# Optimization experiments

Hardware: AMD Instinct MI355X
Metric: run time of the kernel (lower is better)

## Reference

```python
import jax, jax.numpy as jnp
import numpy as np
from jax import lax

# ---- module constants (mirror CorrelatedSphericalField.__init__) ----
NLAT = 361
NLON = 2 * NLAT
LMAX = NLAT            # number of degrees l
MMAX = NLAT + 1        # number of orders m = nlon//2 + 1
N_LATENT = 16
T_STEPS = 8
LENGTH_SCALE = 500_000.0
TIME_SCALE = 48.0
SIGMA = 0.3
DT = 6.0
R_EARTH = 6_371_000.0
PHI = float(np.exp(-DT / TIME_SCALE))
KT = (LENGTH_SCALE / R_EARTH) ** 2 / 2.0
FOUR_PI = float(4.0 * np.pi)


def _precompute_pct():
    """Associated Legendre tensor pct[m, l, k] for InverseRealSHT,
    equiangular grid, norm='backward' (orthonormal P / sqrt(4pi)), with
    Condon-Shortley phase -- matches torch_harmonics _precompute_legpoly(inverse=True)."""
    theta = np.linspace(0.0, np.pi, NLAT)      # equiangular incl. poles
    x = np.cos(theta)
    s = np.sin(theta)
    nmax = max(MMAX, LMAX)
    vdm = np.zeros((nmax, nmax, NLAT), dtype=np.float64)  # [m, l, lat]
    vdm[0, 0] = 1.0 / np.sqrt(4.0 * np.pi)
    for m in range(1, nmax):                    # diagonal P_m^m
        vdm[m, m] = np.sqrt((2.0 * m + 1.0) / (2.0 * m)) * s * vdm[m - 1, m - 1]
    for m in range(nmax - 1):                   # P_{m+1}^m
        vdm[m, m + 1] = np.sqrt(2.0 * m + 3.0) * x * vdm[m, m]
    for l in range(2, nmax):                    # three-term recurrence, vectorized over m
        ms = np.arange(l - 1)
        a = np.sqrt((4.0 * l * l - 1.0) / (l * l - ms * ms))[:, None]
        b = np.sqrt(((l - 1.0) ** 2 - ms * ms) / (4.0 * (l - 1.0) ** 2 - 1.0))[:, None]
        vdm[ms, l] = a * (x[None, :] * vdm[ms, l - 1] - b * vdm[ms, l - 2])
    vdm[1::2] *= -1.0                           # Condon-Shortley phase
    pct = vdm[:MMAX, :LMAX] / np.sqrt(4.0 * np.pi)  # norm='backward', inverse=True
    return jnp.asarray(pct, dtype=jnp.float32)


def _make_sigma_n():
    j = np.arange(1, NLAT, dtype=np.float64)
    denom = 2.0 * np.sum((2.0 * j + 1.0) * np.exp(-KT * j * (j + 1.0)))
    F0 = np.sqrt(SIGMA ** 2 * (1.0 - PHI ** 2) / denom)
    l = np.arange(NLAT, dtype=np.float64)
    prods = np.repeat((l * (l + 1.0))[:, None], MMAX, axis=1)   # (nlat, nlat+1)
    sn = np.tril(np.exp(-KT * prods / 2.0) * F0)                # keep m <= l
    return jnp.asarray(sn, dtype=jnp.float32)


def setup_inputs() -> dict:
    key = jax.random.key(0)
    k0, k1 = jax.random.split(key)
    sigma_n = _make_sigma_n()
    # initial stationary AR(1) coefficients: (1-phi^2)^{-1/2} * sigma_n * xi0
    xi0 = jax.random.normal(k0, (N_LATENT, LMAX, MMAX, 2), dtype=jnp.float32)
    coeff0 = (1.0 - PHI ** 2) ** (-0.5) * sigma_n[None, :, :, None] * xi0
    # pre-drawn innovations for the T AR(1) updates (real/imag stacked)
    xi = jax.random.normal(k1, (T_STEPS, N_LATENT, LMAX, MMAX, 2), dtype=jnp.float32)
    pct = _precompute_pct()
    x = jnp.zeros((T_STEPS,), dtype=jnp.int32)   # only x.shape[0] is used
    return {"x": x, "sigma_n": sigma_n, "coeff0": coeff0, "xi": xi, "pct": pct}


def reference(x, sigma_n, coeff0, xi, pct):
    T = x.shape[0]
    c0 = coeff0[..., 0] + 1j * coeff0[..., 1]    # (N, L, M) complex64
    xic = xi[..., 0] + 1j * xi[..., 1]           # (T, N, L, M) complex64

    # AR(1): emit coeff BEFORE update (matches the torch loop ordering)
    def step(c, xk):
        return PHI * c + sigma_n * xk, c

    _, coeffs = lax.scan(step, c0, xic[:T])      # (T, N, L, M)

    # inverse real SHT, batched over all T steps at once:
    # xs[..., k, m] = sum_l coeff[..., l, m] * pct[m, l, k]
    re = jnp.einsum('tnlm,mlk->tnkm', coeffs.real, pct)
    im = jnp.einsum('tnlm,mlk->tnkm', coeffs.imag, pct)
    xs = re + 1j * im                            # (T, N, nlat, mmax)
    out = jnp.fft.irfft(xs, n=NLON, axis=-1, norm='forward') * FOUR_PI
    return out.reshape(T, 1, 1, N_LATENT, NLAT, NLON)
```

## Files before the change

### kernel.cpp

```cpp
#include <hip/hip_runtime.h>
#include <math.h>

#define NLATC   361
#define NLONC   722
#define MMAXC   362
#define LMAXC   361
#define NLK     16
#define TSTEPS  8
#define LCUT    128
#define MCUT    128
#define MCK     256
#define TNK     46208
#define NPAD    768
#define KPAD    384
#define PHI_F   0.8824969025845955f
#define FOURPI  12.566370614359172f
#define ASCALE  1024.0f
#define OSCALE  0.0009765625f

typedef _Float16 half8 __attribute__((ext_vector_type(8)));
typedef float floatx4 __attribute__((ext_vector_type(4)));

__global__ __launch_bounds__(256) void k_basis2(_Float16* __restrict__ Bf) {
    int idx = blockIdx.x * 256 + threadIdx.x;
    int j = idx >> 8, mc = idx & 255;
    int m = mc >> 1, c = mc & 1;
    float v = 0.0f;
    if (j < NLONC) {
        int r = (m * j) % NLONC;
        float th = (float)r * (6.283185307179586f / 722.0f);
        float s, co;
        sincosf(th, &s, &co);
        float wq = (m == 0 ? 1.0f : 2.0f) * FOURPI;
        v = c ? (-wq * s) : (wq * co);
    }
    Bf[idx] = (_Float16)v;
}

__global__ __launch_bounds__(256) void k_scan(const float* __restrict__ coeff0,
                                              const float* __restrict__ sigma_n,
                                              const float* __restrict__ xi,
                                              float* __restrict__ cA) {
    int tid = blockIdx.x * 256 + threadIdx.x;
    int m = tid & 127;
    int l = (tid >> 7) & 127;
    int n = tid >> 14;
    float sg = sigma_n[(size_t)l * MMAXC + m];
    const float* c0p = coeff0 + (((size_t)n * LMAXC + l) * MMAXC + m) * 2;
    float cr = c0p[0], ci = c0p[1];
#pragma unroll
    for (int t = 0; t < TSTEPS; ++t) {
        size_t o = ((((size_t)t * NLK + n) * LCUT + l) * MCUT + m) * 2;
        cA[o] = cr; cA[o + 1] = ci;
        if (t < TSTEPS - 1) {
            const float* xp = xi + ((((size_t)t * NLK + n) * LMAXC + l) * MMAXC + m) * 2;
            cr = PHI_F * cr + sg * xp[0];
            ci = PHI_F * ci + sg * xp[1];
        }
    }
}

__global__ __launch_bounds__(256) void k_castA(const float* __restrict__ cA,
                                               _Float16* __restrict__ cB) {
    __shared__ _Float16 sm[64][66];
    int tx = threadIdx.x & 63, ty = threadIdx.x >> 6;
    int tnl0 = blockIdx.x * 64;
    int mc0  = blockIdx.y * 64;
    int tn = tnl0 >> 7, l0 = tnl0 & 127;
#pragma unroll
    for (int i = 0; i < 16; ++i) {
        int row = ty * 16 + i;
        sm[row][tx] = (_Float16)(cA[(size_t)(tnl0 + row) * MCK + mc0 + tx] * ASCALE);
    }
    __syncthreads();
#pragma unroll
    for (int i = 0; i < 16; ++i) {
        int rm = ty * 16 + i;
        int mc = mc0 + rm, m = mc >> 1, c = mc & 1;
        cB[((size_t)m * 256 + c * 128 + tn) * 128 + l0 + tx] = sm[tx][rm];
    }
}

__global__ __launch_bounds__(256) void k_transP(const float* __restrict__ pct,
                                                _Float16* __restrict__ pTf) {
    __shared__ _Float16 sm[64][66];
    int tx = threadIdx.x & 63, ty = threadIdx.x >> 6;
    int k0 = blockIdx.x * 64;
    int l0 = blockIdx.y * 64;
    int m  = blockIdx.z;
#pragma unroll
    for (int i = 0; i < 16; ++i) {
        int row = ty * 16 + i;
        int k = k0 + tx;
        sm[row][tx] = (k < NLATC)
            ? (_Float16)pct[((size_t)m * LMAXC + l0 + row) * NLATC + k] : (_Float16)0.0f;
    }
    __syncthreads();
#pragma unroll
    for (int i = 0; i < 16; ++i) {
        int kr = ty * 16 + i;
        pTf[((size_t)m * KPAD + k0 + kr) * 128 + l0 + tx] = sm[tx][kr];
    }
}

__global__ __launch_bounds__(256) void k_leg(const _Float16* __restrict__ cB,
                                             const _Float16* __restrict__ pTf,
                                             _Float16* __restrict__ xsTh) {
    __shared__ _Float16 As[256][40];
    __shared__ _Float16 Bs[64][40];
    int tid = threadIdx.x;
    int k0c = blockIdx.x * 64;
    int m   = blockIdx.y;
    int w = tid >> 6, lane = tid & 63, m16 = lane & 15, quad = lane >> 4;
    floatx4 acc[4][4];
#pragma unroll
    for (int i = 0; i < 4; ++i)
#pragma unroll
        for (int j = 0; j < 4; ++j) acc[i][j] = (floatx4)(0.0f);

    int lt0 = m & ~31;
    for (int lt = lt0; lt < 128; lt += 32) {
#pragma unroll
        for (int it = 0; it < 4; ++it) {
            int r = (tid >> 2) + 64 * it, lc = (tid & 3) * 8;
            *(half8*)&As[r][lc] = *(const half8*)&cB[((size_t)m * 256 + r) * 128 + lt + lc];
        }
        {
            int k = tid >> 2, lc = (tid & 3) * 8;
            *(half8*)&Bs[k][lc] = *(const half8*)&pTf[((size_t)m * KPAD + k0c + k) * 128 + lt + lc];
        }
        __syncthreads();
        half8 a[4], b[4];
#pragma unroll
        for (int i = 0; i < 4; ++i) a[i] = *(const half8*)&As[w * 64 + i * 16 + m16][quad * 8];
#pragma unroll
        for (int j = 0; j < 4; ++j) b[j] = *(const half8*)&Bs[j * 16 + m16][quad * 8];
#pragma unroll
        for (int i = 0; i < 4; ++i)
#pragma unroll
            for (int j = 0; j < 4; ++j)
                acc[i][j] = __builtin_amdgcn_mfma_f32_16x16x32_f16(a[i], b[j], acc[i][j], 0, 0, 0);
        __syncthreads();
    }
#pragma unroll
    for (int i = 0; i < 4; ++i)
#pragma unroll
        for (int j = 0; j < 4; ++j)
#pragma unroll
            for (int reg = 0; reg < 4; ++reg) {
                int r = w * 64 + i * 16 + quad * 4 + reg;
                int c = r >> 7, tn = r & 127;
                int k = k0c + j * 16 + m16;
                if (k < NLATC)
                    xsTh[(size_t)(2 * m + c) * TNK + tn * NLATC + k] = (_Float16)acc[i][j][reg];
            }
}

__global__ __launch_bounds__(256) void k_castXs(const _Float16* __restrict__ xsTh,
                                                _Float16* __restrict__ xsA) {
    __shared__ _Float16 sm[64][66];
    int tx = threadIdx.x & 63, ty = threadIdx.x >> 6;
    int t0  = blockIdx.x * 64;
    int mc0 = blockIdx.y * 64;
#pragma unroll
    for (int i = 0; i < 16; ++i) {
        int row = ty * 16 + i;
        sm[row][tx] = xsTh[(size_t)(mc0 + row) * TNK + t0 + tx];
    }
    __syncthreads();
#pragma unroll
    for (int i = 0; i < 16; ++i) {
        int row = ty * 16 + i;
        xsA[(size_t)(t0 + row) * MCK + mc0 + tx] = sm[tx][row];
    }
}

__global__ __launch_bounds__(256) void k_gemm2(const _Float16* __restrict__ A,
                                               const _Float16* __restrict__ Bf,
                                               float* __restrict__ C) {
    __shared__ _Float16 As[128][40];
    __shared__ _Float16 Bs[128][40];
    int tid = threadIdx.x;
    int row0 = blockIdx.x * 128;
    int j0   = blockIdx.y * 128;
    int w = tid >> 6, lane = tid & 63, m16 = lane & 15, quad = lane >> 4;
    int wr = (w & 1) * 64, wc = (w >> 1) * 64;
    floatx4 acc[4][4];
#pragma unroll
    for (int i = 0; i < 4; ++i)
#pragma unroll
        for (int j = 0; j < 4; ++j) acc[i][j] = (floatx4)(0.0f);

    for (int k0 = 0; k0 < MCK; k0 += 32) {
#pragma unroll
        for (int it = 0; it < 2; ++it) {
            int r = (tid >> 2) + 64 * it, kc = (tid & 3) * 8;
            *(half8*)&As[r][kc] = *(const half8*)&A[(size_t)(row0 + r) * MCK + k0 + kc];
            *(half8*)&Bs[r][kc] = *(const half8*)&Bf[(size_t)(j0 + r) * MCK + k0 + kc];
        }
        __syncthreads();
        half8 a[4], b[4];
#pragma unroll
        for (int i = 0; i < 4; ++i) a[i] = *(const half8*)&As[wr + i * 16 + m16][quad * 8];
#pragma unroll
        for (int j = 0; j < 4; ++j) b[j] = *(const half8*)&Bs[wc + j * 16 + m16][quad * 8];
#pragma unroll
        for (int i = 0; i < 4; ++i)
#pragma unroll
            for (int j = 0; j < 4; ++j)
                acc[i][j] = __builtin_amdgcn_mfma_f32_16x16x32_f16(a[i], b[j], acc[i][j], 0, 0, 0);
        __syncthreads();
    }
#pragma unroll
    for (int i = 0; i < 4; ++i)
#pragma unroll
        for (int j = 0; j < 4; ++j)
#pragma unroll
            for (int reg = 0; reg < 4; ++reg) {
                int row = row0 + wr + i * 16 + quad * 4 + reg;
                int col = j0 + wc + j * 16 + m16;
                if (col < NLONC)
                    C[(size_t)row * NLONC + col] = acc[i][j][reg] * OSCALE;
            }
}

extern "C" void kernel_launch(void* const* d_in, const int* in_sizes, int n_in,
                              void* d_out, int out_size, void* d_ws, size_t ws_size,
                              hipStream_t stream) {
    (void)in_sizes; (void)n_in; (void)out_size; (void)ws_size;
    const float* sigma_n = (const float*)d_in[1];
    const float* coeff0  = (const float*)d_in[2];
    const float* xi      = (const float*)d_in[3];
    const float* pct     = (const float*)d_in[4];
    float* out = (float*)d_out;

    char* ws = (char*)d_ws;
    size_t off = 0;
    float*    cA   = (float*)(ws + off);    off += (size_t)128 * 128 * MCK * 4;
    _Float16* cB   = (_Float16*)(ws + off); off += (size_t)128 * 256 * 128 * 2;
    _Float16* pTf  = (_Float16*)(ws + off); off += (size_t)128 * KPAD * 128 * 2;
    _Float16* xsTh = (_Float16*)(ws + off); off += (size_t)MCK * TNK * 2;
    _Float16* xsA  = (_Float16*)(ws + off); off += (size_t)TNK * MCK * 2;
    _Float16* Bf   = (_Float16*)(ws + off); off += (size_t)NPAD * MCK * 2;

    k_basis2<<<NPAD, 256, 0, stream>>>(Bf);
    k_scan<<<(NLK * LCUT * MCUT) / 256, 256, 0, stream>>>(coeff0, sigma_n, xi, cA);
    k_castA<<<dim3(256, 4), 256, 0, stream>>>(cA, cB);
    k_transP<<<dim3(6, 2, 128), 256, 0, stream>>>(pct, pTf);
    k_leg<<<dim3(6, 128), 256, 0, stream>>>(cB, pTf, xsTh);
    k_castXs<<<dim3(722, 4), 256, 0, stream>>>(xsTh, xsA);
    k_gemm2<<<dim3(361, 6), 256, 0, stream>>>(xsA, Bf, out);
}
```

Before: 421.6 us.

## Merge basis, scan, cast and pct transpose into one prep kernel

Combines the four preprocessing kernels into a single launch whose block ranges cover Fourier basis generation, pct transposition, and the AR(1) scan. The scan now writes fp16 coefficients directly in the transposed layout that the Legendre GEMM consumes, using vectorized half8 stores. This drops the fp32 intermediate buffer and the separate cast/transpose pass. It removes three launches and a global round-trip, but the scan blocks now read xi with a strided pattern of 8 l-rows per thread.

Measured after the change: 416.0 us. No clear change (-1.3%).

```diff
diff --git a/kernel.cpp b/kernel.cpp
--- a/kernel.cpp
+++ b/kernel.cpp
@@ -21,85 +21,86 @@
 typedef _Float16 half8 __attribute__((ext_vector_type(8)));
 typedef float floatx4 __attribute__((ext_vector_type(4)));
 
-__global__ __launch_bounds__(256) void k_basis2(_Float16* __restrict__ Bf) {
-    int idx = blockIdx.x * 256 + threadIdx.x;
-    int j = idx >> 8, mc = idx & 255;
-    int m = mc >> 1, c = mc & 1;
-    float v = 0.0f;
-    if (j < NLONC) {
-        int r = (m * j) % NLONC;
-        float th = (float)r * (6.283185307179586f / 722.0f);
-        float s, co;
-        sincosf(th, &s, &co);
-        float wq = (m == 0 ? 1.0f : 2.0f) * FOURPI;
-        v = c ? (-wq * s) : (wq * co);
-    }
-    Bf[idx] = (_Float16)v;
-}
-
-__global__ __launch_bounds__(256) void k_scan(const float* __restrict__ coeff0,
-                                              const float* __restrict__ sigma_n,
+__global__ __launch_bounds__(256) void k_prep(const float* __restrict__ sigma_n,
+                                              const float* __restrict__ coeff0,
                                               const float* __restrict__ xi,
-                                              float* __restrict__ cA) {
-    int tid = blockIdx.x * 256 + threadIdx.x;
-    int m = tid & 127;
-    int l = (tid >> 7) & 127;
-    int n = tid >> 14;
-    float sg = sigma_n[(size_t)l * MMAXC + m];
-    const float* c0p = coeff0 + (((size_t)n * LMAXC + l) * MMAXC + m) * 2;
-    float cr = c0p[0], ci = c0p[1];
-#pragma unroll
-    for (int t = 0; t < TSTEPS; ++t) {
-        size_t o = ((((size_t)t * NLK + n) * LCUT + l) * MCUT + m) * 2;
-        cA[o] = cr; cA[o + 1] = ci;
-        if (t < TSTEPS - 1) {
-            const float* xp = xi + ((((size_t)t * NLK + n) * LMAXC + l) * MMAXC + m) * 2;
-            cr = PHI_F * cr + sg * xp[0];
-            ci = PHI_F * ci + sg * xp[1];
-        }
-    }
-}
-
-__global__ __launch_bounds__(256) void k_castA(const float* __restrict__ cA,
-                                               _Float16* __restrict__ cB) {
+                                              const float* __restrict__ pct,
+                                              _Float16* __restrict__ Bf,
+                                              _Float16* __restrict__ pTf,
+                                              _Float16* __restrict__ cB) {
     __shared__ _Float16 sm[64][66];
-    int tx = threadIdx.x & 63, ty = threadIdx.x >> 6;
-    int tnl0 = blockIdx.x * 64;
-    int mc0  = blockIdx.y * 64;
-    int tn = tnl0 >> 7, l0 = tnl0 & 127;
-#pragma unroll
-    for (int i = 0; i < 16; ++i) {
-        int row = ty * 16 + i;
-        sm[row][tx] = (_Float16)(cA[(size_t)(tnl0 + row) * MCK + mc0 + tx] * ASCALE);
-    }
-    __syncthreads();
-#pragma unroll
-    for (int i = 0; i < 16; ++i) {
-        int rm = ty * 16 + i;
-        int mc = mc0 + rm, m = mc >> 1, c = mc & 1;
-        cB[((size_t)m * 256 + c * 128 + tn) * 128 + l0 + tx] = sm[tx][rm];
-    }
-}
-
-__global__ __launch_bounds__(256) void k_transP(const float* __restrict__ pct,
-                                                _Float16* __restrict__ pTf) {
-    __shared__ _Float16 sm[64][66];
-    int tx = threadIdx.x & 63, ty = threadIdx.x >> 6;
-    int k0 = blockIdx.x * 64;
-    int l0 = blockIdx.y * 64;
-    int m  = blockIdx.z;
-#pragma unroll
-    for (int i = 0; i < 16; ++i) {
-        int row = ty * 16 + i;
-        int k = k0 + tx;
-        sm[row][tx] = (k < NLATC)
-            ? (_Float16)pct[((size_t)m * LMAXC + l0 + row) * NLATC + k] : (_Float16)0.0f;
-    }
-    __syncthreads();
-#pragma unroll
-    for (int i = 0; i < 16; ++i) {
-        int kr = ty * 16 + i;
-        pTf[((size_t)m * KPAD + k0 + kr) * 128 + l0 + tx] = sm[tx][kr];
+    int bid = blockIdx.x;
+    int tid = threadIdx.x;
+
+    if (bid < 768) {
+        int idx = bid * 256 + tid;
+        int j = idx >> 8, mc = idx & 255;
+        int m = mc >> 1, c = mc & 1;
+        float v = 0.0f;
+        if (j < NLONC) {
+            int r = (m * j) % NLONC;
+            float th = (float)r * (6.283185307179586f / 722.0f);
+            float s, co;
+            sincosf(th, &s, &co);
+            float wq = (m == 0 ? 1.0f : 2.0f) * FOURPI;
+            v = c ? (-wq * s) : (wq * co);
+        }
+        Bf[idx] = (_Float16)v;
+    } else if (bid < 2304) {
+        int b = bid - 768;
+        int k0 = (b % 6) * 64;
+        int l0 = ((b / 6) & 1) * 64;
+        int m  = b / 12;
+        int tx = tid & 63, ty = tid >> 6;
+#pragma unroll
+        for (int i = 0; i < 16; ++i) {
+            int row = ty * 16 + i;
+            int k = k0 + tx;
+            sm[row][tx] = (k < NLATC)
+                ? (_Float16)pct[((size_t)m * LMAXC + l0 + row) * NLATC + k] : (_Float16)0.0f;
+        }
+        __syncthreads();
+#pragma unroll
+        for (int i = 0; i < 16; ++i) {
+            int kr = ty * 16 + i;
+            pTf[((size_t)m * KPAD + k0 + kr) * 128 + l0 + tx] = sm[tx][kr];
+        }
+    } else {
+        int b = bid - 2304;
+        int mt = b & 3, lt = (b >> 2) & 1, n = b >> 3;
+        int ml = tid & 31, lg = tid >> 5;
+        int m  = mt * 32 + ml;
+        int l0 = lt * 64 + lg * 8;
+        float cr[8], ci[8], sg[8];
+#pragma unroll
+        for (int i = 0; i < 8; ++i) {
+            int l = l0 + i;
+            sg[i] = sigma_n[(size_t)l * MMAXC + m];
+            float2 c0 = *(const float2*)&coeff0[(((size_t)n * LMAXC + l) * MMAXC + m) * 2];
+            cr[i] = c0.x; ci[i] = c0.y;
+        }
+#pragma unroll
+        for (int t = 0; t < TSTEPS; ++t) {
+            half8 hr, hi;
+#pragma unroll
+            for (int i = 0; i < 8; ++i) {
+                hr[i] = (_Float16)(cr[i] * ASCALE);
+                hi[i] = (_Float16)(ci[i] * ASCALE);
+            }
+            size_t rowR = ((size_t)m * 256 +       t * 16 + n) * 128 + l0;
+            size_t rowI = ((size_t)m * 256 + 128 + t * 16 + n) * 128 + l0;
+            *(half8*)&cB[rowR] = hr;
+            *(half8*)&cB[rowI] = hi;
+            if (t < TSTEPS - 1) {
+#pragma unroll
+                for (int i = 0; i < 8; ++i) {
+                    float2 x = *(const float2*)
+                        &xi[((((size_t)t * NLK + n) * LMAXC + l0 + i) * MMAXC + m) * 2];
+                    cr[i] = PHI_F * cr[i] + sg[i] * x.x;
+                    ci[i] = PHI_F * ci[i] + sg[i] * x.y;
+                }
+            }
+        }
     }
 }
 
@@ -236,17 +237,13 @@
 
     char* ws = (char*)d_ws;
     size_t off = 0;
-    float*    cA   = (float*)(ws + off);    off += (size_t)128 * 128 * MCK * 4;
     _Float16* cB   = (_Float16*)(ws + off); off += (size_t)128 * 256 * 128 * 2;
     _Float16* pTf  = (_Float16*)(ws + off); off += (size_t)128 * KPAD * 128 * 2;
     _Float16* xsTh = (_Float16*)(ws + off); off += (size_t)MCK * TNK * 2;
     _Float16* xsA  = (_Float16*)(ws + off); off += (size_t)TNK * MCK * 2;
     _Float16* Bf   = (_Float16*)(ws + off); off += (size_t)NPAD * MCK * 2;
 
-    k_basis2<<<NPAD, 256, 0, stream>>>(Bf);
-    k_scan<<<(NLK * LCUT * MCUT) / 256, 256, 0, stream>>>(coeff0, sigma_n, xi, cA);
-    k_castA<<<dim3(256, 4), 256, 0, stream>>>(cA, cB);
-    k_transP<<<dim3(6, 2, 128), 256, 0, stream>>>(pct, pTf);
+    k_prep<<<2432, 256, 0, stream>>>(sigma_n, coeff0, xi, pct, Bf, pTf, cB);
     k_leg<<<dim3(6, 128), 256, 0, stream>>>(cB, pTf, xsTh);
     k_castXs<<<dim3(722, 4), 256, 0, stream>>>(xsTh, xsA);
     k_gemm2<<<dim3(361, 6), 256, 0, stream>>>(xsA, Bf, out);
```
